# Optimization experiments

Measured on AMD Instinct MI355X. Metric: run time of the kernel, lower is better.

Reference implementation:

```python
import jax, jax.numpy as jnp
import numpy as np

HIDDEN = 1024
VOCAB = 128000

def setup_inputs() -> dict:
    key = jax.random.key(0)
    ks = jax.random.split(key, 9)
    s = 0.02
    return {
        "seq_input": jax.random.randint(ks[0], (1,), 0, VOCAB),
        "hidden": jax.random.normal(ks[1], (1, 1, HIDDEN), dtype=jnp.float32),
        "emb": jax.random.normal(ks[2], (VOCAB, HIDDEN), dtype=jnp.float32) * s,
        "w_ih": jax.random.normal(ks[3], (3 * HIDDEN, HIDDEN), dtype=jnp.float32) * s,
        "w_hh": jax.random.normal(ks[4], (3 * HIDDEN, HIDDEN), dtype=jnp.float32) * s,
        "b_ih": jax.random.normal(ks[5], (3 * HIDDEN,), dtype=jnp.float32) * s,
        "b_hh": jax.random.normal(ks[6], (3 * HIDDEN,), dtype=jnp.float32) * s,
        "w_out": jax.random.normal(ks[7], (VOCAB, HIDDEN), dtype=jnp.float32) * s,
        "b_out": jax.random.normal(ks[8], (VOCAB,), dtype=jnp.float32) * s,
    }

def reference(seq_input, hidden, emb, w_ih, w_hh, b_ih, b_hh, w_out, b_out):
    # embedding lookup + relu: [1, H]
    x = jax.nn.relu(emb[seq_input])
    h = hidden[0]  # [1, H] (num_layers=1, batch=1)
    # single-step GRU (PyTorch gate ordering: r, z, n)
    gi = x @ w_ih.T + b_ih     # [1, 3H]
    gh = h @ w_hh.T + b_hh     # [1, 3H]
    i_r, i_z, i_n = jnp.split(gi, 3, axis=-1)
    h_r, h_z, h_n = jnp.split(gh, 3, axis=-1)
    r = jax.nn.sigmoid(i_r + h_r)
    z = jax.nn.sigmoid(i_z + h_z)
    n = jnp.tanh(i_n + r * h_n)
    h_new = (1.0 - z) * n + z * h  # [1, H]
    # output projection + log-softmax over vocab: [1, V]
    logits = h_new @ w_out.T + b_out
    logprobs = jax.nn.log_softmax(logits, axis=1)
    return logprobs, h_new[None]  # hidden back to [1,1,H]
```

## Files before the change

### kernel.cpp

```cpp
#include <hip/hip_runtime.h>

#define H 1024
#define V 128000
#define NBLK_LOGITS 2000

#define WS_GI   0
#define WS_GH   3072
#define WS_PART 6144

__device__ __forceinline__ float wave_sum(float acc) {
    #pragma unroll
    for (int m = 32; m >= 1; m >>= 1) acc += __shfl_xor(acc, m);
    return acc;
}

__device__ __forceinline__ void online_combine(float& m, float& s, float om, float os) {
    const float M = fmaxf(m, om);
    s = s * expf(m - M) + os * expf(om - M);
    m = M;
}

__global__ void gates_kernel(const int* __restrict__ seq,
                             const float* __restrict__ hidden,
                             const float* __restrict__ emb,
                             const float* __restrict__ w_ih,
                             const float* __restrict__ w_hh,
                             const float* __restrict__ b_ih,
                             const float* __restrict__ b_hh,
                             float* __restrict__ ws) {
    const int wid  = threadIdx.x >> 6;
    const int lane = threadIdx.x & 63;
    const int row  = blockIdx.x * 4 + wid;
    if (row >= 6144) return;
    const int idx = seq[0];

    const float* wrow;
    const float* v;
    float bias;
    bool relu_in;
    if (row < 3072) {
        wrow = w_ih + (size_t)row * H;
        v    = emb + (size_t)idx * H;
        bias = b_ih[row];
        relu_in = true;
    } else {
        const int r = row - 3072;
        wrow = w_hh + (size_t)r * H;
        v    = hidden;
        bias = b_hh[r];
        relu_in = false;
    }

    float acc = 0.f;
    #pragma unroll
    for (int k = 0; k < 4; ++k) {
        const int j = lane * 4 + k * 256;
        float4 wv = *(const float4*)(wrow + j);
        float4 vv = *(const float4*)(v + j);
        if (relu_in) {
            vv.x = fmaxf(vv.x, 0.f); vv.y = fmaxf(vv.y, 0.f);
            vv.z = fmaxf(vv.z, 0.f); vv.w = fmaxf(vv.w, 0.f);
        }
        acc += wv.x * vv.x + wv.y * vv.y + wv.z * vv.z + wv.w * vv.w;
    }
    acc = wave_sum(acc);
    if (lane == 0) ws[row] = acc + bias;
}

__global__ void __launch_bounds__(256) logits_kernel(
        const float* __restrict__ hidden,
        const float* __restrict__ w_out,
        const float* __restrict__ b_out,
        float* __restrict__ ws,
        float* __restrict__ out) {
    __shared__ float sh_h[H];
    __shared__ float sm[4], ssum[4];
    const int tid = threadIdx.x;

    #pragma unroll
    for (int k = 0; k < 4; ++k) {
        const int i = tid + k * 256;
        const float gi_r = ws[WS_GI + i];
        const float gi_z = ws[WS_GI + H + i];
        const float gi_n = ws[WS_GI + 2 * H + i];
        const float gh_r = ws[WS_GH + i];
        const float gh_z = ws[WS_GH + H + i];
        const float gh_n = ws[WS_GH + 2 * H + i];
        const float r = 1.f / (1.f + expf(-(gi_r + gh_r)));
        const float z = 1.f / (1.f + expf(-(gi_z + gh_z)));
        const float n = tanhf(gi_n + r * gh_n);
        const float h = hidden[i];
        sh_h[i] = (1.f - z) * n + z * h;
    }
    __syncthreads();

    if (blockIdx.x == 0) {
        #pragma unroll
        for (int k = 0; k < 4; ++k) {
            const int i = tid + k * 256;
            out[V + i] = sh_h[i];
        }
    }

    const int wid  = tid >> 6;
    const int lane = tid & 63;
    float4 hv[4];
    #pragma unroll
    for (int k = 0; k < 4; ++k) hv[k] = *(const float4*)(&sh_h[lane * 4 + k * 256]);

    float m = -1e30f, s = 0.f;
    const int nwaves = NBLK_LOGITS * 4;
    for (int row = blockIdx.x * 4 + wid; row < V; row += nwaves) {
        const float* wr = w_out + (size_t)row * H;
        float acc = 0.f;
        #pragma unroll
        for (int k = 0; k < 4; ++k) {
            float4 wv = *(const float4*)(wr + lane * 4 + k * 256);
            acc += wv.x * hv[k].x + wv.y * hv[k].y + wv.z * hv[k].z + wv.w * hv[k].w;
        }
        acc = wave_sum(acc) + b_out[row];
        if (lane == 0) out[row] = acc;
        if (acc > m) { s = s * expf(m - acc) + 1.f; m = acc; }
        else         { s += expf(acc - m); }
    }

    if (lane == 0) { sm[wid] = m; ssum[wid] = s; }
    __syncthreads();
    if (tid == 0) {
        float M = sm[0], S = ssum[0];
        #pragma unroll
        for (int w = 1; w < 4; ++w) online_combine(M, S, sm[w], ssum[w]);
        ws[WS_PART + 2 * blockIdx.x]     = M;
        ws[WS_PART + 2 * blockIdx.x + 1] = S;
    }
}

__global__ void smax_write(float* __restrict__ out, const float* __restrict__ ws) {
    const int tid  = threadIdx.x;
    const int wid  = tid >> 6;
    const int lane = tid & 63;
    __shared__ float sm[4], ssum[4];
    __shared__ float c_sh;

    float m = -1e30f, s = 0.f;
    for (int i = tid; i < NBLK_LOGITS; i += 256) {
        online_combine(m, s, ws[WS_PART + 2 * i], ws[WS_PART + 2 * i + 1]);
    }
    #pragma unroll
    for (int d = 1; d < 64; d <<= 1) {
        const float om = __shfl_xor(m, d);
        const float os = __shfl_xor(s, d);
        online_combine(m, s, om, os);
    }
    if (lane == 0) { sm[wid] = m; ssum[wid] = s; }
    __syncthreads();
    if (tid == 0) {
        float M = sm[0], S = ssum[0];
        #pragma unroll
        for (int w = 1; w < 4; ++w) online_combine(M, S, sm[w], ssum[w]);
        c_sh = M + logf(S);
    }
    __syncthreads();
    const float c = c_sh;

    const int i = (blockIdx.x * 256 + tid) * 4;
    float4 v = *(float4*)(out + i);
    v.x -= c; v.y -= c; v.z -= c; v.w -= c;
    *(float4*)(out + i) = v;
}

extern "C" void kernel_launch(void* const* d_in, const int* in_sizes, int n_in,
                              void* d_out, int out_size, void* d_ws, size_t ws_size,
                              hipStream_t stream) {
    const int*   seq    = (const int*)d_in[0];
    const float* hidden = (const float*)d_in[1];
    const float* emb    = (const float*)d_in[2];
    const float* w_ih   = (const float*)d_in[3];
    const float* w_hh   = (const float*)d_in[4];
    const float* b_ih   = (const float*)d_in[5];
    const float* b_hh   = (const float*)d_in[6];
    const float* w_out  = (const float*)d_in[7];
    const float* b_out  = (const float*)d_in[8];
    float* out = (float*)d_out;
    float* ws  = (float*)d_ws;

    gates_kernel<<<1536, 256, 0, stream>>>(seq, hidden, emb, w_ih, w_hh, b_ih, b_hh, ws);
    logits_kernel<<<NBLK_LOGITS, 256, 0, stream>>>(hidden, w_out, b_out, ws, out);
    smax_write<<<125, 256, 0, stream>>>(out, ws);
}
```

Before: 111.6 us.

## Fuse log-softmax normalization into logits kernel via grid-wide atomic barrier

Removes the separate softmax-write kernel. The logits kernel now keeps 32 logits per wave in registers, synchronizes all 1000 blocks through an atomic counter barrier, reduces the partial max/sum, and writes the normalized log-probs directly. This avoids a second pass over the 128000-float output and one kernel launch. The cost is a memset launch for the counter, a grid barrier that can deadlock if not all 1000 blocks are co-resident, and higher register pressure from the fully unrolled row loop.

Result: slower. 425.5 us (+281.4%).

```diff
diff --git a/kernel.cpp b/kernel.cpp
--- a/kernel.cpp
+++ b/kernel.cpp
@@ -2,11 +2,13 @@
 
 #define H 1024
 #define V 128000
-#define NBLK_LOGITS 2000
+#define NBLK_FUSED 1000
+#define ROWS_PER_WAVE 32
 
 #define WS_GI   0
 #define WS_GH   3072
 #define WS_PART 6144
+#define WS_BAR  8192
 
 __device__ __forceinline__ float wave_sum(float acc) {
     #pragma unroll
@@ -67,7 +69,7 @@
     if (lane == 0) ws[row] = acc + bias;
 }
 
-__global__ void __launch_bounds__(256) logits_kernel(
+__global__ void __launch_bounds__(256, 4) logits_kernel(
         const float* __restrict__ hidden,
         const float* __restrict__ w_out,
         const float* __restrict__ b_out,
@@ -75,7 +77,10 @@
         float* __restrict__ out) {
     __shared__ float sh_h[H];
     __shared__ float sm[4], ssum[4];
-    const int tid = threadIdx.x;
+    __shared__ float c_sh;
+    const int tid  = threadIdx.x;
+    const int wid  = tid >> 6;
+    const int lane = tid & 63;
 
     #pragma unroll
     for (int k = 0; k < 4; ++k) {
@@ -102,24 +107,24 @@
         }
     }
 
-    const int wid  = tid >> 6;
-    const int lane = tid & 63;
     float4 hv[4];
     #pragma unroll
     for (int k = 0; k < 4; ++k) hv[k] = *(const float4*)(&sh_h[lane * 4 + k * 256]);
 
+    const int row0 = (blockIdx.x * 4 + wid) * ROWS_PER_WAVE;
+    float lg[ROWS_PER_WAVE];
     float m = -1e30f, s = 0.f;
-    const int nwaves = NBLK_LOGITS * 4;
-    for (int row = blockIdx.x * 4 + wid; row < V; row += nwaves) {
-        const float* wr = w_out + (size_t)row * H;
+    #pragma unroll
+    for (int r = 0; r < ROWS_PER_WAVE; ++r) {
+        const float* wr = w_out + (size_t)(row0 + r) * H;
         float acc = 0.f;
         #pragma unroll
         for (int k = 0; k < 4; ++k) {
             float4 wv = *(const float4*)(wr + lane * 4 + k * 256);
             acc += wv.x * hv[k].x + wv.y * hv[k].y + wv.z * hv[k].z + wv.w * hv[k].w;
         }
-        acc = wave_sum(acc) + b_out[row];
-        if (lane == 0) out[row] = acc;
+        acc = wave_sum(acc) + b_out[row0 + r];
+        lg[r] = acc;
         if (acc > m) { s = s * expf(m - acc) + 1.f; m = acc; }
         else         { s += expf(acc - m); }
     }
@@ -133,26 +138,31 @@
         ws[WS_PART + 2 * blockIdx.x]     = M;
         ws[WS_PART + 2 * blockIdx.x + 1] = S;
     }
-}
-
-__global__ void smax_write(float* __restrict__ out, const float* __restrict__ ws) {
-    const int tid  = threadIdx.x;
-    const int wid  = tid >> 6;
-    const int lane = tid & 63;
-    __shared__ float sm[4], ssum[4];
-    __shared__ float c_sh;
-
-    float m = -1e30f, s = 0.f;
-    for (int i = tid; i < NBLK_LOGITS; i += 256) {
-        online_combine(m, s, ws[WS_PART + 2 * i], ws[WS_PART + 2 * i + 1]);
+
+    __threadfence();
+    __syncthreads();
+    unsigned* bar = (unsigned*)&ws[WS_BAR];
+    if (tid == 0) {
+        __hip_atomic_fetch_add(bar, 1u, __ATOMIC_ACQ_REL, __HIP_MEMORY_SCOPE_AGENT);
+        while (__hip_atomic_load(bar, __ATOMIC_RELAXED, __HIP_MEMORY_SCOPE_AGENT)
+               < (unsigned)NBLK_FUSED) {
+            __builtin_amdgcn_s_sleep(2);
+        }
+    }
+    __syncthreads();
+    __threadfence();
+
+    float rm = -1e30f, rs = 0.f;
+    for (int i = tid; i < NBLK_FUSED; i += 256) {
+        online_combine(rm, rs, ws[WS_PART + 2 * i], ws[WS_PART + 2 * i + 1]);
     }
     #pragma unroll
     for (int d = 1; d < 64; d <<= 1) {
-        const float om = __shfl_xor(m, d);
-        const float os = __shfl_xor(s, d);
-        online_combine(m, s, om, os);
-    }
-    if (lane == 0) { sm[wid] = m; ssum[wid] = s; }
+        const float om = __shfl_xor(rm, d);
+        const float os = __shfl_xor(rs, d);
+        online_combine(rm, rs, om, os);
+    }
+    if (lane == 0) { sm[wid] = rm; ssum[wid] = rs; }
     __syncthreads();
     if (tid == 0) {
         float M = sm[0], S = ssum[0];
@@ -163,10 +173,12 @@
     __syncthreads();
     const float c = c_sh;
 
-    const int i = (blockIdx.x * 256 + tid) * 4;
-    float4 v = *(float4*)(out + i);
-    v.x -= c; v.y -= c; v.z -= c; v.w -= c;
-    *(float4*)(out + i) = v;
+    if (lane == 0) {
+        #pragma unroll
+        for (int r = 0; r < ROWS_PER_WAVE; ++r) {
+            out[row0 + r] = lg[r] - c;
+        }
+    }
 }
 
 extern "C" void kernel_launch(void* const* d_in, const int* in_sizes, int n_in,
@@ -184,7 +196,7 @@
     float* out = (float*)d_out;
     float* ws  = (float*)d_ws;
 
+    hipMemsetAsync(ws + WS_BAR, 0, sizeof(unsigned), stream);
     gates_kernel<<<1536, 256, 0, stream>>>(seq, hidden, emb, w_ih, w_hh, b_ih, b_hh, ws);
-    logits_kernel<<<NBLK_LOGITS, 256, 0, stream>>>(hidden, w_out, b_out, ws, out);
-    smax_write<<<125, 256, 0, stream>>>(out, ws);
-}
+    logits_kernel<<<NBLK_FUSED, 256, 0, stream>>>(hidden, w_out, b_out, ws, out);
+}
```

## Move softmax stats out of logits GEMV into separate partial-reduction kernel

Applied to the files above, without the earlier changes.

The logits kernel now gives each wave a contiguous block of 16 rows, fully unrolled, with the bias fetched once per wave and broadcast by shuffle. The online softmax update is removed from the GEMV loop, and a new smax_partial kernel rereads the logits to compute per-block max and sum. Fast __expf and an exp-based tanh replace the precise functions, and occupancy hints are added. The cost is an extra kernel launch plus a 512KB reread of the logits, and slightly lower numerical accuracy.

Result: slower. 115.2 us (+3.3%).

```diff
diff --git a/kernel.cpp b/kernel.cpp
--- a/kernel.cpp
+++ b/kernel.cpp
@@ -3,6 +3,7 @@
 #define H 1024
 #define V 128000
 #define NBLK_LOGITS 2000
+#define NBLK_SMAX 125
 
 #define WS_GI   0
 #define WS_GH   3072
@@ -16,7 +17,7 @@
 
 __device__ __forceinline__ void online_combine(float& m, float& s, float om, float os) {
     const float M = fmaxf(m, om);
-    s = s * expf(m - M) + os * expf(om - M);
+    s = s * __expf(m - M) + os * __expf(om - M);
     m = M;
 }
 
@@ -67,14 +68,13 @@
     if (lane == 0) ws[row] = acc + bias;
 }
 
-__global__ void __launch_bounds__(256) logits_kernel(
+__global__ void __launch_bounds__(256, 8) logits_kernel(
         const float* __restrict__ hidden,
         const float* __restrict__ w_out,
         const float* __restrict__ b_out,
-        float* __restrict__ ws,
+        const float* __restrict__ ws,
         float* __restrict__ out) {
     __shared__ float sh_h[H];
-    __shared__ float sm[4], ssum[4];
     const int tid = threadIdx.x;
 
     #pragma unroll
@@ -86,9 +86,11 @@
         const float gh_r = ws[WS_GH + i];
         const float gh_z = ws[WS_GH + H + i];
         const float gh_n = ws[WS_GH + 2 * H + i];
-        const float r = 1.f / (1.f + expf(-(gi_r + gh_r)));
-        const float z = 1.f / (1.f + expf(-(gi_z + gh_z)));
-        const float n = tanhf(gi_n + r * gh_n);
+        const float r = 1.f / (1.f + __expf(-(gi_r + gh_r)));
+        const float z = 1.f / (1.f + __expf(-(gi_z + gh_z)));
+        const float a = gi_n + r * gh_n;
+        const float e2 = __expf(2.f * a);
+        const float n = 1.f - 2.f / (e2 + 1.f);
         const float h = hidden[i];
         sh_h[i] = (1.f - z) * n + z * h;
     }
@@ -108,22 +110,41 @@
     #pragma unroll
     for (int k = 0; k < 4; ++k) hv[k] = *(const float4*)(&sh_h[lane * 4 + k * 256]);
 
-    float m = -1e30f, s = 0.f;
-    const int nwaves = NBLK_LOGITS * 4;
-    for (int row = blockIdx.x * 4 + wid; row < V; row += nwaves) {
-        const float* wr = w_out + (size_t)row * H;
+    const int row0 = (blockIdx.x * 4 + wid) * 16;
+    const float myb = (lane < 16) ? b_out[row0 + lane] : 0.f;
+
+    #pragma unroll
+    for (int t = 0; t < 16; ++t) {
+        const float* wr = w_out + (size_t)(row0 + t) * H;
         float acc = 0.f;
         #pragma unroll
         for (int k = 0; k < 4; ++k) {
-            float4 wv = *(const float4*)(wr + lane * 4 + k * 256);
+            const int j = lane * 4 + k * 256;
+            float4 wv = *(const float4*)(wr + j);
             acc += wv.x * hv[k].x + wv.y * hv[k].y + wv.z * hv[k].z + wv.w * hv[k].w;
         }
-        acc = wave_sum(acc) + b_out[row];
-        if (lane == 0) out[row] = acc;
-        if (acc > m) { s = s * expf(m - acc) + 1.f; m = acc; }
-        else         { s += expf(acc - m); }
-    }
-
+        acc = wave_sum(acc) + __shfl(myb, t);
+        if (lane == 0) out[row0 + t] = acc;
+    }
+}
+
+__global__ void smax_partial(const float* __restrict__ out, float* __restrict__ ws) {
+    const int tid  = threadIdx.x;
+    const int wid  = tid >> 6;
+    const int lane = tid & 63;
+    __shared__ float sm[4], ssum[4];
+
+    const int i = (blockIdx.x * 256 + tid) * 4;
+    const float4 v = *(const float4*)(out + i);
+    float m = fmaxf(fmaxf(v.x, v.y), fmaxf(v.z, v.w));
+    float s = __expf(v.x - m) + __expf(v.y - m) + __expf(v.z - m) + __expf(v.w - m);
+
+    #pragma unroll
+    for (int d = 1; d < 64; d <<= 1) {
+        const float om = __shfl_xor(m, d);
+        const float os = __shfl_xor(s, d);
+        online_combine(m, s, om, os);
+    }
     if (lane == 0) { sm[wid] = m; ssum[wid] = s; }
     __syncthreads();
     if (tid == 0) {
@@ -143,8 +164,9 @@
     __shared__ float c_sh;
 
     float m = -1e30f, s = 0.f;
-    for (int i = tid; i < NBLK_LOGITS; i += 256) {
-        online_combine(m, s, ws[WS_PART + 2 * i], ws[WS_PART + 2 * i + 1]);
+    if (tid < NBLK_SMAX) {
+        m = ws[WS_PART + 2 * tid];
+        s = ws[WS_PART + 2 * tid + 1];
     }
     #pragma unroll
     for (int d = 1; d < 64; d <<= 1) {
@@ -186,5 +208,6 @@
 
     gates_kernel<<<1536, 256, 0, stream>>>(seq, hidden, emb, w_ih, w_hh, b_ih, b_hh, ws);
     logits_kernel<<<NBLK_LOGITS, 256, 0, stream>>>(hidden, w_out, b_out, ws, out);
-    smax_write<<<125, 256, 0, stream>>>(out, ws);
-}
+    smax_partial<<<NBLK_SMAX, 256, 0, stream>>>(out, ws);
+    smax_write<<<NBLK_SMAX, 256, 0, stream>>>(out, ws);
+}
```
